# Optimization experiments

Hardware: AMD Instinct MI355X
Metric: run time of the kernel (lower is better)

The kernel has to match this reference:

```python
import jax, jax.numpy as jnp
import numpy as np
from jax import lax

V = 32000   # vocab_size
H = 1024    # hidden_size
B = 32      # batch
S = 64      # encoder (source) length
T = 64      # decoder (target) length


def setup_inputs() -> dict:
    key = jax.random.key(0)
    ks = jax.random.split(key, 16)
    scale = 0.05

    def p(k, shape):
        return jax.random.normal(k, shape, dtype=jnp.float32) * scale

    input_seqs = jax.random.randint(ks[0], (B, S), 0, V)
    target_seqs = jax.random.randint(ks[1], (B, T), 0, V)
    # pack_padded_sequence requires descending-sorted lengths >= 1
    input_lens = jnp.sort(jax.random.randint(ks[2], (B,), S // 2, S + 1))[::-1].astype(jnp.int32)

    return {
        "input_seqs": input_seqs,
        "target_seqs": target_seqs,
        "input_lens": input_lens,
        # encoder params (torch GRU layout: gates [r|z|n] stacked on first dim)
        "emb_enc": p(ks[3], (V, H)),
        "W_ih_e": p(ks[4], (3 * H, H)),
        "W_hh_e": p(ks[5], (3 * H, H)),
        "b_ih_e": p(ks[6], (3 * H,)),
        "b_hh_e": p(ks[7], (3 * H,)),
        # decoder params (GRU input size is 2H due to [embedded ; thought] concat)
        "emb_dec": p(ks[8], (V, H)),
        "W_ih_d": p(ks[9], (3 * H, 2 * H)),
        "W_hh_d": p(ks[10], (3 * H, H)),
        "b_ih_d": p(ks[11], (3 * H,)),
        "b_hh_d": p(ks[12], (3 * H,)),
        "W_out": p(ks[13], (V, H)),
        "b_out": p(ks[14], (V,)),
    }


def _gru_step(xp_t, h, W_hh, b_hh):
    """One torch-style GRU step. xp_t = x_t @ W_ih.T + b_ih, shape [B, 3H]."""
    gh = h @ W_hh.T + b_hh                     # [B, 3H]
    xr, xz, xn = jnp.split(xp_t, 3, axis=-1)
    hr, hz, hn = jnp.split(gh, 3, axis=-1)
    r = jax.nn.sigmoid(xr + hr)
    z = jax.nn.sigmoid(xz + hz)
    n = jnp.tanh(xn + r * hn)
    return (1.0 - z) * n + z * h


def reference(input_seqs, target_seqs, input_lens,
              emb_enc, W_ih_e, W_hh_e, b_ih_e, b_hh_e,
              emb_dec, W_ih_d, W_hh_d, b_ih_d, b_hh_d,
              W_out, b_out):
    b, s = input_seqs.shape
    t = target_seqs.shape[1]
    h_dim = emb_enc.shape[1]

    # ---------------- Encoder (packed GRU == masked recurrence) ----------------
    x = emb_enc[input_seqs]                                   # [B, S, H]
    xp = jnp.einsum('bsh,gh->bsg', x, W_ih_e) + b_ih_e        # [B, S, 3H], all input projs at once
    valid = jnp.arange(s)[:, None] < input_lens[None, :]      # [S, B]

    def enc_step(h, inp):
        xp_t, m_t = inp                                       # [B,3H], [B]
        h_new = _gru_step(xp_t, h, W_hh_e, b_hh_e)
        # packed sequence: hidden frozen past each row's true length
        return jnp.where(m_t[:, None], h_new, h), None

    h0 = jnp.zeros((b, h_dim), dtype=x.dtype)
    thought, _ = lax.scan(enc_step, h0, (xp.transpose(1, 0, 2), valid))  # [B, H]

    # ---------------- Decoder ----------------
    e = emb_dec[target_seqs]                                  # [B, T, H]
    # create_rnn_input: broadcast-concat thought onto every timestep
    rnn_in = jnp.concatenate(
        [e, jnp.broadcast_to(thought[:, None, :], (b, t, h_dim))], axis=-1)  # [B, T, 2H]
    rnn_in = jax.nn.relu(rnn_in)                              # F.relu before the GRU
    xp_d = jnp.einsum('bsh,gh->bsg', rnn_in, W_ih_d) + b_ih_d # [B, T, 3H]

    def dec_step(h, xp_t):
        h_new = _gru_step(xp_t, h, W_hh_d, b_hh_d)
        return h_new, h_new

    h0d = jnp.zeros((b, h_dim), dtype=e.dtype)                # decoder init_hidden = zeros
    _, hs = lax.scan(dec_step, h0d, xp_d.transpose(1, 0, 2))  # [T, B, H]

    logits = jnp.einsum('tbh,vh->tbv', hs, W_out) + b_out     # [T, B, V]
    log_probs = jax.nn.log_softmax(logits, axis=-1)           # softmax_batch == per-row log_softmax
    return log_probs.transpose(1, 0, 2)                       # [B, T, V]
```

## Files before the change

### kernel.cpp

```cpp
#include <hip/hip_runtime.h>
#include <stdint.h>
#include <stddef.h>

#define VOCAB 32000
#define HID   1024
#define NB    32
#define SLEN  64
#define TLEN  64
#define G3    3072

typedef float          f32x4  __attribute__((ext_vector_type(4)));
typedef float          f32x2  __attribute__((ext_vector_type(2)));
typedef __bf16         bf16x8 __attribute__((ext_vector_type(8)));
typedef unsigned short u16x8  __attribute__((ext_vector_type(8)));
typedef unsigned short u16x4  __attribute__((ext_vector_type(4)));
typedef unsigned int   u32x4  __attribute__((ext_vector_type(4)));

union BfPun { u16x8 u; bf16x8 b; };
union CvPun { u32x4 u; bf16x8 b; };

__device__ __forceinline__ unsigned short f2bf(float f) {
  unsigned int u = __builtin_bit_cast(unsigned int, f);
  u += 0x7FFFu + ((u >> 16) & 1u);
  return (unsigned short)(u >> 16);
}
__device__ __forceinline__ float bf2f(unsigned short h) {
  unsigned int u = (unsigned int)h << 16;
  return __builtin_bit_cast(float, u);
}

__device__ __forceinline__ float sig_f(float x) {
  return __builtin_amdgcn_rcpf(1.f + __expf(-x));
}
__device__ __forceinline__ float tanh_f(float x) {
  return 2.f * __builtin_amdgcn_rcpf(1.f + __expf(-2.f * x)) - 1.f;
}

__device__ __forceinline__ void gld_lds16(const unsigned short* g, unsigned short* l) {
  __builtin_amdgcn_global_load_lds(
      (const __attribute__((address_space(1))) unsigned int*)g,
      (__attribute__((address_space(3))) unsigned int*)l,
      16, 0, 0);
}


__global__ __launch_bounds__(256) void cvt_bf16(const float* __restrict__ in,
                                                unsigned short* __restrict__ out) {
  size_t idx = ((size_t)blockIdx.x * 256 + threadIdx.x) * 4;
  f32x4 v = *(const f32x4*)(in + idx);
  u16x4 o;
  o[0] = f2bf(v[0]); o[1] = f2bf(v[1]); o[2] = f2bf(v[2]); o[3] = f2bf(v[3]);
  *(u16x4*)(out + idx) = o;
}

__global__ __launch_bounds__(256) void cvt_split_d(const float* __restrict__ Wd,
                                                   unsigned short* __restrict__ W1,
                                                   unsigned short* __restrict__ W2) {
  int r = blockIdx.x, q = threadIdx.x;
  const float* src = Wd + (size_t)r * 2048;
  f32x4 v1 = *(const f32x4*)(src + q * 4);
  f32x4 v2 = *(const f32x4*)(src + 1024 + q * 4);
  u16x4 o1, o2;
  o1[0]=f2bf(v1[0]); o1[1]=f2bf(v1[1]); o1[2]=f2bf(v1[2]); o1[3]=f2bf(v1[3]);
  o2[0]=f2bf(v2[0]); o2[1]=f2bf(v2[1]); o2[2]=f2bf(v2[2]); o2[3]=f2bf(v2[3]);
  *(u16x4*)(W1 + (size_t)r * 1024 + q * 4) = o1;
  *(u16x4*)(W2 + (size_t)r * 1024 + q * 4) = o2;
}

__global__ __launch_bounds__(128) void cvt_whh_frag(const float* __restrict__ W,
                                                    unsigned short* __restrict__ Wv) {
  int r = blockIdx.x;
  int g = r >> 10, i = r & 1023, blk = i >> 4, il = i & 15;
  int q = threadIdx.x;
  int ks = q >> 2, ksub = q & 3, lane = il + ksub * 16;
  f32x4 v0 = *(const f32x4*)(W + (size_t)r * HID + q * 8);
  f32x4 v1 = *(const f32x4*)(W + (size_t)r * HID + q * 8 + 4);
  u16x8 o;
  o[0]=f2bf(v0[0]); o[1]=f2bf(v0[1]); o[2]=f2bf(v0[2]); o[3]=f2bf(v0[3]);
  o[4]=f2bf(v1[0]); o[5]=f2bf(v1[1]); o[6]=f2bf(v1[2]); o[7]=f2bf(v1[3]);
  size_t dst = ((((size_t)blk * 3 + g) * 32 + ks) * 64 + lane) * 8;
  *(u16x8*)(Wv + dst) = o;
}

__global__ __launch_bounds__(256) void gather_embed(const int* __restrict__ seqs,
                                                    const float* __restrict__ emb,
                                                    unsigned short* __restrict__ Aout,
                                                    int relu) {
  int r = blockIdx.x, q = threadIdx.x;
  int tok = seqs[r];
  f32x4 v = *(const f32x4*)(emb + (size_t)tok * HID + q * 4);
  if (relu) {
    v[0]=fmaxf(v[0],0.f); v[1]=fmaxf(v[1],0.f); v[2]=fmaxf(v[2],0.f); v[3]=fmaxf(v[3],0.f);
  }
  u16x4 o; o[0]=f2bf(v[0]); o[1]=f2bf(v[1]); o[2]=f2bf(v[2]); o[3]=f2bf(v[3]);
  *(u16x4*)(Aout + (size_t)r * HID + q * 4) = o;
}

__global__ __launch_bounds__(256) void gather_thought(const float* __restrict__ hfin,
                                                      unsigned short* __restrict__ Aout) {
  int r = blockIdx.x, q = threadIdx.x;
  u16x4 o = {0, 0, 0, 0};
  if (r < NB) {
    f32x4 v = *(const f32x4*)(hfin + (size_t)r * HID + q * 4);
    o[0]=f2bf(fmaxf(v[0],0.f)); o[1]=f2bf(fmaxf(v[1],0.f));
    o[2]=f2bf(fmaxf(v[2],0.f)); o[3]=f2bf(fmaxf(v[3],0.f));
  }
  *(u16x4*)(Aout + (size_t)r * HID + q * 4) = o;
}

__global__ __launch_bounds__(256) void zero_f32(float* __restrict__ p) {
  p[blockIdx.x * 256 + threadIdx.x] = 0.f;
}

template<int MODE, int MT>
__global__ __launch_bounds__(256) void gemm_bf16(const unsigned short* __restrict__ A,
                                                 const unsigned short* __restrict__ Bw,
                                                 const float* __restrict__ bias,
                                                 const float* __restrict__ add2,
                                                 void* __restrict__ outv, int N) {
  __shared__ unsigned short Abuf[128 * 64];
  __shared__ unsigned short Bbuf[128 * 64];
  const int K = HID;
  int tid = threadIdx.x, lane = tid & 63, wid = tid >> 6;
  int nwg = gridDim.x;
  int u = (blockIdx.x & 7) * (nwg >> 3) + (blockIdx.x >> 3);
  int g = u / (MT * 4);
  int r_ = u - g * (MT * 4);
  int bm = r_ % MT;
  int bn = g * 4 + r_ / MT;
  int wrow = wid >> 1, wcol = wid & 1;
  f32x4 zero4 = {0.f, 0.f, 0.f, 0.f};
  f32x4 acc[4][4];
#pragma unroll
  for (int i = 0; i < 4; ++i)
#pragma unroll
    for (int j = 0; j < 4; ++j) acc[i][j] = zero4;

  int srow = tid >> 3;
  int csrc = (tid & 7) ^ (srow & 7);
  const unsigned short* Ag = A + ((size_t)bm * 128 + srow) * K + csrc * 8;
  const unsigned short* Bg = Bw + ((size_t)bn * 128 + srow) * K + csrc * 8;
  unsigned short* As = Abuf + tid * 8;
  unsigned short* Bs = Bbuf + tid * 8;

  int ca0 = (0 * 4 + (lane >> 4)) ^ (lane & 7);
  int ca1 = (1 * 4 + (lane >> 4)) ^ (lane & 7);

  for (int ks = 0; ks < 16; ++ks) {
    size_t k0 = ks * 64;
    __syncthreads();
#pragma unroll
    for (int j = 0; j < 4; ++j)
      gld_lds16(Ag + (size_t)j * 32 * K + k0, As + j * 2048);
#pragma unroll
    for (int j = 0; j < 4; ++j)
      gld_lds16(Bg + (size_t)j * 32 * K + k0, Bs + j * 2048);
    __syncthreads();
#pragma unroll
    for (int kk = 0; kk < 2; ++kk) {
      int cc = kk ? ca1 : ca0;
      bf16x8 af[4], bfr[4];
#pragma unroll
      for (int mi = 0; mi < 4; ++mi) {
        BfPun tpun;
        tpun.u = *(const u16x8*)(Abuf + (wrow * 64 + mi * 16 + (lane & 15)) * 64 + cc * 8);
        af[mi] = tpun.b;
      }
#pragma unroll
      for (int ni = 0; ni < 4; ++ni) {
        BfPun tpun;
        tpun.u = *(const u16x8*)(Bbuf + (wcol * 64 + ni * 16 + (lane & 15)) * 64 + cc * 8);
        bfr[ni] = tpun.b;
      }
#pragma unroll
      for (int mi = 0; mi < 4; ++mi)
#pragma unroll
        for (int ni = 0; ni < 4; ++ni)
          acc[mi][ni] = __builtin_amdgcn_mfma_f32_16x16x32_bf16(af[mi], bfr[ni], acc[mi][ni], 0, 0, 0);
    }
  }

  float* out = (float*)outv;
  unsigned short* o16 = (unsigned short*)outv;
#pragma unroll
  for (int mi = 0; mi < 4; ++mi) {
    int rb = bm * 128 + wrow * 64 + mi * 16 + ((lane >> 4) << 2);
#pragma unroll
    for (int ni = 0; ni < 4; ++ni) {
      int c = bn * 128 + wcol * 64 + ni * 16 + (lane & 15);
#pragma unroll
      for (int e = 0; e < 4; ++e) {
        int r = rb + e;
        float v = acc[mi][ni][e];
        if (MODE == 0) {
          out[(size_t)r * N + c] = v + bias[c];
        } else if (MODE == 1) {
          int t = r & 63, b = r >> 6;
          int gg = c >> 10, ci = c & 1023;
          out[(((size_t)t * 3 + gg) * NB + b) * HID + ci] = v + bias[c];
        } else if (MODE == 2) {
          int t = r & 63, b = r >> 6;
          int gg = c >> 10, ci = c & 1023;
          out[(((size_t)t * 3 + gg) * NB + b) * HID + ci] = v + add2[(size_t)b * G3 + c];
        } else {
          int b = r & 31, t = r >> 5;
          o16[(size_t)(b * 64 + t) * (VOCAB * 2) + c] = f2bf(v + bias[c]);
        }
      }
    }
  }
}

__global__ __launch_bounds__(384, 1) void gru_scan(
    const unsigned short* __restrict__ Wv,
    const float* __restrict__ b_hh,
    const float* __restrict__ xpT,
    unsigned short* __restrict__ hbx,
    const int* __restrict__ lens,
    unsigned short* __restrict__ hs_out,
    float* __restrict__ hfin,
    int* __restrict__ bar, int nsteps) {
  __shared__ unsigned short Wlds[49152];
  __shared__ float gh[48][33];
  __shared__ float h32[32][16];
  __shared__ float bhh_s[48];
  __shared__ int   lens_s[32];
  int tid = threadIdx.x, lane = tid & 63, w = tid >> 6;
  int g = w >> 1, part = w & 1;
  int blk = blockIdx.x, i0 = blk * 16;

  if (tid < 32) lens_s[tid] = lens ? lens[tid] : 0x7fffffff;
  if (tid >= 64 && tid < 112) {
    int q = tid - 64;
    bhh_s[q] = b_hh[(size_t)(q >> 4) * HID + i0 + (q & 15)];
  }
  if (tid < 256) h32[tid >> 3][((tid & 7) * 2)] = 0.f;
  if (tid < 256) h32[tid >> 3][((tid & 7) * 2) + 1] = 0.f;

  {
    const unsigned short* Wsrc = Wv + (size_t)blk * 49152;
    for (int j = tid; j < 6144; j += 384)
      *(u16x8*)(Wlds + (size_t)j * 8) = *(const u16x8*)(Wsrc + (size_t)j * 8);
  }
  __syncthreads();

  int eb = tid >> 3, eil = (tid & 7) * 2;
  f32x2 xr2, xz2, xn2;

  for (int t = 0; t < nsteps; ++t) {
    if (tid < 256) {
      const float* xb = xpT + ((size_t)t * 3 * NB + eb) * HID + i0 + eil;
      xr2 = *(const f32x2*)(xb);
      xz2 = *(const f32x2*)(xb + (size_t)NB * HID);
      xn2 = *(const f32x2*)(xb + (size_t)2 * NB * HID);
    }
    f32x4 acc = {0.f, 0.f, 0.f, 0.f};
    if (t > 0) {
      const unsigned short* hp = hbx + (size_t)(t - 1) * 32768 + part * 16384 + lane * 8;
      u32x4 pb[16];
#pragma unroll
      for (int j = 0; j < 16; ++j) pb[j] = *(const u32x4*)(hp + (size_t)j * 512);
#pragma unroll
      for (int ks = 0; ks < 32; ++ks) {
        BfPun a_;
        a_.u = *(const u16x8*)(Wlds + ((size_t)(g * 32 + ks) * 64 + lane) * 8);
        CvPun cv; cv.u = pb[ks & 15];
        if (ks + 16 < 32) pb[ks & 15] = *(const u32x4*)(hp + (size_t)(ks + 16) * 512);
        acc = __builtin_amdgcn_mfma_f32_16x16x32_bf16(a_.b, cv.b, acc, 0, 0, 0);
      }
    }
    {
      int il4 = (lane >> 4) * 4, cb = part * 16 + (lane & 15);
#pragma unroll
      for (int e = 0; e < 4; ++e) gh[g * 16 + il4 + e][cb] = acc[e];
    }
    __syncthreads();

    if (tid < 256) {
      float sr0 = gh[eil][eb],      sr1 = gh[eil + 1][eb];
      float sz0 = gh[16 + eil][eb], sz1 = gh[16 + eil + 1][eb];
      float sn0 = gh[32 + eil][eb], sn1 = gh[32 + eil + 1][eb];
      float rg0 = sig_f(xr2[0] + sr0 + bhh_s[eil]);
      float rg1 = sig_f(xr2[1] + sr1 + bhh_s[eil + 1]);
      float zg0 = sig_f(xz2[0] + sz0 + bhh_s[16 + eil]);
      float zg1 = sig_f(xz2[1] + sz1 + bhh_s[16 + eil + 1]);
      float ng0 = tanh_f(xn2[0] + rg0 * (sn0 + bhh_s[32 + eil]));
      float ng1 = tanh_f(xn2[1] + rg1 * (sn1 + bhh_s[32 + eil + 1]));
      float h0o = h32[eb][eil], h1o = h32[eb][eil + 1];
      float hn0 = (1.f - zg0) * ng0 + zg0 * h0o;
      float hn1 = (1.f - zg1) * ng1 + zg1 * h1o;
      if (t >= lens_s[eb]) { hn0 = h0o; hn1 = h1o; }
      h32[eb][eil] = hn0; h32[eb][eil + 1] = hn1;
      unsigned int pk = (unsigned int)f2bf(hn0) | ((unsigned int)f2bf(hn1) << 16);
      int k = i0 + eil;
      int ksf = k >> 5, lnf = (eb & 15) + ((k >> 3) & 3) * 16, sub = k & 7;
      unsigned short* dst = hbx + (size_t)t * 32768 + (size_t)(eb >> 4) * 16384
                            + (size_t)ksf * 512 + lnf * 8 + sub;
      __hip_atomic_store((unsigned int*)dst, pk, __ATOMIC_RELAXED, __HIP_MEMORY_SCOPE_AGENT);
      if (hs_out)
        *(unsigned int*)(hs_out + ((size_t)t * NB + eb) * HID + k) = pk;
    }

    if (t + 1 < nsteps) {
      __syncthreads();
      if (tid == 0)
        __hip_atomic_fetch_add(&bar[(t * 8 + (blk & 7)) * 16], 1,
                               __ATOMIC_RELAXED, __HIP_MEMORY_SCOPE_AGENT);
      if (tid < 64) {
        const int* cp = &bar[(t * 8 + (lane & 7)) * 16];
        while (__hip_atomic_load(cp, __ATOMIC_RELAXED, __HIP_MEMORY_SCOPE_AGENT) < 8)
          __builtin_amdgcn_s_sleep(1);
      }
      __syncthreads();
    }
  }

  if (hfin && tid < 256) {
    f32x2 hv; hv[0] = h32[eb][eil]; hv[1] = h32[eb][eil + 1];
    *(f32x2*)(hfin + (size_t)eb * HID + i0 + eil) = hv;
  }
}

__global__ __launch_bounds__(1024, 1) void log_softmax_bf16(float* __restrict__ out) {
  __shared__ float rowbuf[VOCAB];
  __shared__ float ms[16], ss[16];
  size_t row = blockIdx.x;
  const unsigned short* src = (const unsigned short*)out + row * (VOCAB * 2);
  int tid = threadIdx.x;
  float m = -3.0e38f, s = 0.f;
  for (int j = tid; j < VOCAB / 8; j += 1024) {
    u16x8 v = *(const u16x8*)(src + j * 8);
#pragma unroll
    for (int e = 0; e < 8; ++e) {
      float x = bf2f(v[e]);
      rowbuf[j * 8 + e] = x;
      float nm = fmaxf(m, x);
      s = s * __expf(m - nm) + __expf(x - nm);
      m = nm;
    }
  }
#pragma unroll
  for (int off = 1; off < 64; off <<= 1) {
    float m2 = __shfl_xor(m, off, 64);
    float s2 = __shfl_xor(s, off, 64);
    float nm = fmaxf(m, m2);
    s = s * __expf(m - nm) + s2 * __expf(m2 - nm);
    m = nm;
  }
  if ((tid & 63) == 0) { ms[tid >> 6] = m; ss[tid >> 6] = s; }
  __syncthreads();
  float M = -3.0e38f;
#pragma unroll
  for (int i = 0; i < 16; ++i) M = fmaxf(M, ms[i]);
  float S = 0.f;
#pragma unroll
  for (int i = 0; i < 16; ++i) S += ss[i] * __expf(ms[i] - M);
  float lse = M + __logf(S);
  f32x4* o4 = (f32x4*)(out + row * VOCAB);
  for (int j = tid; j < VOCAB / 4; j += 1024) {
    f32x4 v = *(const f32x4*)(rowbuf + j * 4);
    v[0] -= lse; v[1] -= lse; v[2] -= lse; v[3] -= lse;
    o4[j] = v;
  }
}


extern "C" void kernel_launch(void* const* d_in, const int* in_sizes, int n_in,
                              void* d_out, int out_size, void* d_ws, size_t ws_size,
                              hipStream_t stream) {
  (void)in_sizes; (void)n_in; (void)out_size; (void)ws_size;
  const int*   input_seqs  = (const int*)d_in[0];
  const int*   target_seqs = (const int*)d_in[1];
  const int*   input_lens  = (const int*)d_in[2];
  const float* emb_enc = (const float*)d_in[3];
  const float* W_ih_e  = (const float*)d_in[4];
  const float* W_hh_e  = (const float*)d_in[5];
  const float* b_ih_e  = (const float*)d_in[6];
  const float* b_hh_e  = (const float*)d_in[7];
  const float* emb_dec = (const float*)d_in[8];
  const float* W_ih_d  = (const float*)d_in[9];
  const float* W_hh_d  = (const float*)d_in[10];
  const float* b_ih_d  = (const float*)d_in[11];
  const float* b_hh_d  = (const float*)d_in[12];
  const float* W_out   = (const float*)d_in[13];
  const float* b_out   = (const float*)d_in[14];
  float* out = (float*)d_out;

  char* p = (char*)d_ws;
  auto take = [&](size_t n) { char* q = p; p += (n + 255) & ~(size_t)255; return q; };
  unsigned short* Wbf_e  = (unsigned short*)take((size_t)G3 * HID * 2);
  unsigned short* Wbf_1d = (unsigned short*)take((size_t)G3 * HID * 2);
  unsigned short* Wbf_2d = (unsigned short*)take((size_t)G3 * HID * 2);
  unsigned short* Wbf_o  = (unsigned short*)take((size_t)VOCAB * HID * 2);
  unsigned short* Wv_e   = (unsigned short*)take((size_t)G3 * HID * 2);
  unsigned short* Wv_d   = (unsigned short*)take((size_t)G3 * HID * 2);
  unsigned short* A_ed   = (unsigned short*)take((size_t)2048 * HID * 2);
  unsigned short* A_th   = (unsigned short*)take((size_t)128 * HID * 2);
  unsigned short* A_hs   = (unsigned short*)take((size_t)2048 * HID * 2);
  float* xpT = (float*)take((size_t)64 * 3 * NB * HID * 4);
  float* t2  = (float*)take((size_t)128 * G3 * 4);
  unsigned short* hbx_e = (unsigned short*)take((size_t)SLEN * NB * HID * 2);
  unsigned short* hbx_d = (unsigned short*)take((size_t)TLEN * NB * HID * 2);
  int*   bar_e = (int*)take((size_t)SLEN * 8 * 16 * 4);
  int*   bar_d = (int*)take((size_t)TLEN * 8 * 16 * 4);
  float* hfin = (float*)take((size_t)NB * HID * 4);

  cvt_bf16<<<dim3((G3 * HID) / 1024), 256, 0, stream>>>(W_ih_e, Wbf_e);
  cvt_split_d<<<dim3(G3), 256, 0, stream>>>(W_ih_d, Wbf_1d, Wbf_2d);
  cvt_bf16<<<dim3((VOCAB * HID) / 1024), 256, 0, stream>>>(W_out, Wbf_o);
  cvt_whh_frag<<<dim3(G3), 128, 0, stream>>>(W_hh_e, Wv_e);
  cvt_whh_frag<<<dim3(G3), 128, 0, stream>>>(W_hh_d, Wv_d);
  zero_f32<<<dim3(64), 256, 0, stream>>>((float*)bar_e);

  gather_embed<<<dim3(NB * SLEN), 256, 0, stream>>>(input_seqs, emb_enc, A_ed, 0);
  gemm_bf16<1, 16><<<dim3(384), 256, 0, stream>>>(A_ed, Wbf_e, b_ih_e, nullptr, xpT, G3);
  gru_scan<<<dim3(64), 384, 0, stream>>>(Wv_e, b_hh_e, xpT, hbx_e, input_lens,
                                         nullptr, hfin, bar_e, SLEN);

  gather_thought<<<dim3(128), 256, 0, stream>>>(hfin, A_th);
  gemm_bf16<0, 1><<<dim3(24), 256, 0, stream>>>(A_th, Wbf_2d, b_ih_d, nullptr, t2, G3);
  gather_embed<<<dim3(NB * TLEN), 256, 0, stream>>>(target_seqs, emb_dec, A_ed, 1);
  gemm_bf16<2, 16><<<dim3(384), 256, 0, stream>>>(A_ed, Wbf_1d, nullptr, t2, xpT, G3);

  gru_scan<<<dim3(64), 384, 0, stream>>>(Wv_d, b_hh_d, xpT, hbx_d, nullptr,
                                         A_hs, nullptr, bar_d, TLEN);

  gemm_bf16<3, 16><<<dim3(4000), 256, 0, stream>>>(A_hs, Wbf_o, b_out, nullptr, out, VOCAB);
  log_softmax_bf16<<<dim3(NB * TLEN), 1024, 0, stream>>>(out);
}
```

Before: 870.4 us.

## Add dedicated 256x256-tile double-buffered GEMM for output logits projection

Replaces the generic 128x128-tile GEMM used for the 2048x32000x1024 logits projection with a specialized kernel. It uses 256x256 tiles, 512 threads, double-buffered LDS with direct global-to-LDS loads, and XOR-swizzled LDS layout. MFMA phases are interleaved with prefetch under s_setprio, and blocks are remapped for L2 locality. Larger tiles raise arithmetic intensity and halve redundant A/B reads, at the cost of single-block occupancy and higher register pressure.

```diff
diff --git a/kernel.cpp b/kernel.cpp
--- a/kernel.cpp
+++ b/kernel.cpp
@@ -181,7 +181,6 @@
   }
 
   float* out = (float*)outv;
-  unsigned short* o16 = (unsigned short*)outv;
 #pragma unroll
   for (int mi = 0; mi < 4; ++mi) {
     int rb = bm * 128 + wrow * 64 + mi * 16 + ((lane >> 4) << 2);
@@ -198,14 +197,160 @@
           int t = r & 63, b = r >> 6;
           int gg = c >> 10, ci = c & 1023;
           out[(((size_t)t * 3 + gg) * NB + b) * HID + ci] = v + bias[c];
-        } else if (MODE == 2) {
+        } else {
           int t = r & 63, b = r >> 6;
           int gg = c >> 10, ci = c & 1023;
           out[(((size_t)t * 3 + gg) * NB + b) * HID + ci] = v + add2[(size_t)b * G3 + c];
-        } else {
-          int b = r & 31, t = r >> 5;
-          o16[(size_t)(b * 64 + t) * (VOCAB * 2) + c] = f2bf(v + bias[c]);
         }
+      }
+    }
+  }
+}
+
+__global__ __launch_bounds__(512, 1) void gemm_logits(const unsigned short* __restrict__ A,
+                                                      const unsigned short* __restrict__ Bw,
+                                                      const float* __restrict__ bias,
+                                                      unsigned short* __restrict__ o16) {
+  __shared__ unsigned short Al[2][16384];
+  __shared__ unsigned short Bl[2][16384];
+  const int K = HID;
+  int tid = threadIdx.x, lane = tid & 63, wid = tid >> 6;
+  int wm = wid >> 2, wn = wid & 3;
+  int u = (blockIdx.x & 7) * 125 + (blockIdx.x >> 3);
+  int bm = u & 7, bn = u >> 3;
+
+  f32x4 acc[8][4];
+  f32x4 zero4 = {0.f, 0.f, 0.f, 0.f};
+#pragma unroll
+  for (int a = 0; a < 8; ++a)
+#pragma unroll
+    for (int ni = 0; ni < 4; ++ni) acc[a][ni] = zero4;
+
+  int srow = tid >> 3;
+  int csrc = (tid & 7) ^ (srow & 7);
+  const unsigned short* Ag = A + ((size_t)bm * 256 + srow) * K + csrc * 8;
+  const unsigned short* Bg = Bw + ((size_t)bn * 256 + srow) * K + csrc * 8;
+
+  int arow = wm * 128 + (lane & 15);
+  int bcol = wn * 64 + (lane & 15);
+  int ch0 = (lane >> 4) ^ (lane & 7);
+  int ch1 = ((lane >> 4) + 4) ^ (lane & 7);
+
+#pragma unroll
+  for (int j = 0; j < 4; ++j) gld_lds16(Ag + (size_t)j * 64 * K, &Al[0][j * 4096 + tid * 8]);
+#pragma unroll
+  for (int j = 0; j < 4; ++j) gld_lds16(Bg + (size_t)j * 64 * K, &Bl[0][j * 4096 + tid * 8]);
+  asm volatile("s_waitcnt vmcnt(0)" ::: "memory");
+  __builtin_amdgcn_s_barrier();
+
+  bf16x8 afr[4][2], bf0[2][2], bf1[2][2];
+
+  for (int it = 0; it < 16; ++it) {
+    int cur = it & 1, nxt = cur ^ 1;
+    bool stage = (it < 15);
+    size_t kof = (size_t)(it + 1) * 64;
+    const unsigned short* Ac = &Al[cur][0];
+    const unsigned short* Bc = &Bl[cur][0];
+
+#pragma unroll
+    for (int mi = 0; mi < 4; ++mi) {
+      BfPun t0, t1;
+      t0.u = *(const u16x8*)(Ac + (arow + mi * 16) * 64 + ch0 * 8);
+      t1.u = *(const u16x8*)(Ac + (arow + mi * 16) * 64 + ch1 * 8);
+      afr[mi][0] = t0.b; afr[mi][1] = t1.b;
+    }
+#pragma unroll
+    for (int ni = 0; ni < 2; ++ni) {
+      BfPun t0, t1;
+      t0.u = *(const u16x8*)(Bc + (bcol + ni * 16) * 64 + ch0 * 8);
+      t1.u = *(const u16x8*)(Bc + (bcol + ni * 16) * 64 + ch1 * 8);
+      bf0[ni][0] = t0.b; bf0[ni][1] = t1.b;
+    }
+    if (stage) {
+#pragma unroll
+      for (int j = 0; j < 4; ++j)
+        gld_lds16(Ag + kof + (size_t)j * 64 * K, &Al[nxt][j * 4096 + tid * 8]);
+    }
+    __builtin_amdgcn_s_barrier();
+    __builtin_amdgcn_s_setprio(1);
+#pragma unroll
+    for (int mi = 0; mi < 4; ++mi)
+#pragma unroll
+      for (int ni = 0; ni < 2; ++ni)
+#pragma unroll
+        for (int ks = 0; ks < 2; ++ks)
+          acc[mi][ni] = __builtin_amdgcn_mfma_f32_16x16x32_bf16(afr[mi][ks], bf0[ni][ks], acc[mi][ni], 0, 0, 0);
+    __builtin_amdgcn_s_setprio(0);
+    __builtin_amdgcn_s_barrier();
+
+#pragma unroll
+    for (int ni = 0; ni < 2; ++ni) {
+      BfPun t0, t1;
+      t0.u = *(const u16x8*)(Bc + (bcol + (ni + 2) * 16) * 64 + ch0 * 8);
+      t1.u = *(const u16x8*)(Bc + (bcol + (ni + 2) * 16) * 64 + ch1 * 8);
+      bf1[ni][0] = t0.b; bf1[ni][1] = t1.b;
+    }
+    if (stage) {
+#pragma unroll
+      for (int j = 0; j < 4; ++j)
+        gld_lds16(Bg + kof + (size_t)j * 64 * K, &Bl[nxt][j * 4096 + tid * 8]);
+    }
+    __builtin_amdgcn_s_barrier();
+    __builtin_amdgcn_s_setprio(1);
+#pragma unroll
+    for (int mi = 0; mi < 4; ++mi)
+#pragma unroll
+      for (int ni = 0; ni < 2; ++ni)
+#pragma unroll
+        for (int ks = 0; ks < 2; ++ks)
+          acc[mi][2 + ni] = __builtin_amdgcn_mfma_f32_16x16x32_bf16(afr[mi][ks], bf1[ni][ks], acc[mi][2 + ni], 0, 0, 0);
+    __builtin_amdgcn_s_setprio(0);
+    __builtin_amdgcn_s_barrier();
+
+#pragma unroll
+    for (int mi = 0; mi < 4; ++mi) {
+      BfPun t0, t1;
+      t0.u = *(const u16x8*)(Ac + (arow + 64 + mi * 16) * 64 + ch0 * 8);
+      t1.u = *(const u16x8*)(Ac + (arow + 64 + mi * 16) * 64 + ch1 * 8);
+      afr[mi][0] = t0.b; afr[mi][1] = t1.b;
+    }
+    __builtin_amdgcn_s_barrier();
+    __builtin_amdgcn_s_setprio(1);
+#pragma unroll
+    for (int mi = 0; mi < 4; ++mi)
+#pragma unroll
+      for (int ni = 0; ni < 2; ++ni)
+#pragma unroll
+        for (int ks = 0; ks < 2; ++ks)
+          acc[4 + mi][ni] = __builtin_amdgcn_mfma_f32_16x16x32_bf16(afr[mi][ks], bf0[ni][ks], acc[4 + mi][ni], 0, 0, 0);
+    __builtin_amdgcn_s_setprio(0);
+    __builtin_amdgcn_s_barrier();
+
+    __builtin_amdgcn_s_setprio(1);
+#pragma unroll
+    for (int mi = 0; mi < 4; ++mi)
+#pragma unroll
+      for (int ni = 0; ni < 2; ++ni)
+#pragma unroll
+        for (int ks = 0; ks < 2; ++ks)
+          acc[4 + mi][2 + ni] = __builtin_amdgcn_mfma_f32_16x16x32_bf16(afr[mi][ks], bf1[ni][ks], acc[4 + mi][2 + ni], 0, 0, 0);
+    __builtin_amdgcn_s_setprio(0);
+    if (stage) asm volatile("s_waitcnt vmcnt(0)" ::: "memory");
+    __builtin_amdgcn_s_barrier();
+  }
+
+#pragma unroll
+  for (int a = 0; a < 8; ++a) {
+    int r0 = bm * 256 + wm * 128 + (a >> 2) * 64 + (a & 3) * 16 + ((lane >> 4) << 2);
+#pragma unroll
+    for (int ni = 0; ni < 4; ++ni) {
+      int c = bn * 256 + wn * 64 + ni * 16 + (lane & 15);
+      float bs = bias[c];
+#pragma unroll
+      for (int e = 0; e < 4; ++e) {
+        int r = r0 + e;
+        int b = r & 31, t = r >> 5;
+        o16[(size_t)(b * 64 + t) * (VOCAB * 2) + c] = f2bf(acc[a][ni][e] + bs);
       }
     }
   }
@@ -425,6 +570,6 @@
   gru_scan<<<dim3(64), 384, 0, stream>>>(Wv_d, b_hh_d, xpT, hbx_d, nullptr,
                                          A_hs, nullptr, bar_d, TLEN);
 
-  gemm_bf16<3, 16><<<dim3(4000), 256, 0, stream>>>(A_hs, Wbf_o, b_out, nullptr, out, VOCAB);
+  gemm_logits<<<dim3(1000), 512, 0, stream>>>(A_hs, Wbf_o, b_out, (unsigned short*)out);
   log_softmax_bf16<<<dim3(NB * TLEN), 1024, 0, stream>>>(out);
 }
```

Result: faster. 815.1 us (-6.4%).
